# Optimization experiments

Hardware: AMD Instinct MI355X
Metric: run time of the kernel (lower is better)

## Reference

```python
import jax, jax.numpy as jnp
import numpy as np
from jax import lax

GAMMA = 2        # unused in forward (kept for fidelity to source)
PW = 10.0
THRESHOLD = 1.0
ERODE = 3
BACKZERO = 0

B, C, D, H, W = 2, 1, 128, 256, 256


def setup_inputs() -> dict:
    key = jax.random.key(0)
    k1, k2 = jax.random.split(key)
    inp = jax.random.normal(k1, (B, C, D, H, W), dtype=jnp.float32)
    tgt = jax.random.uniform(k2, (B, C, D, H, W), dtype=jnp.float32)
    return {"input": inp, "target": tgt}


def _box_sum_3d(x, r):
    # All-ones (2r+1)^3 conv3d with padding=r == sliding-window sum (shape-preserving).
    k = 2 * r + 1
    return lax.reduce_window(
        x, 0.0, lax.add,
        window_dimensions=(1, 1, k, k, k),
        window_strides=(1, 1, 1, 1, 1),
        padding=[(0, 0), (0, 0), (r, r), (r, r), (r, r)],
    )


def reference(input, target):
    # weight = clamp(target, 0, threshold); zero out voxels exactly at threshold
    w = jnp.clip(target, 0.0, THRESHOLD)
    w = w - THRESHOLD * (w == THRESHOLD).astype(jnp.float32)
    # box-filter "erosion" then binarize
    w = _box_sum_3d(w, ERODE)
    w = (w > 0).astype(jnp.float32)
    w = 1.0 + w * PW
    if BACKZERO != 0:
        mask = (input < 0).astype(jnp.float32) * (target == 0).astype(jnp.float32)
        w = w * (1.0 - mask)
    loss = jnp.abs(target - input) * w
    return jnp.mean(loss)
```

## Files before the change

### kernel.cpp

```cpp
#include <hip/hip_runtime.h>
#include <stdint.h>

#define BB 2
#define DD 128
#define HH 256
#define WW 256
static constexpr int64_t N = (int64_t)BB * DD * HH * WW;
static constexpr int WPR    = WW / 64;
static constexpr int NWORDS = BB * DD * HH * WPR;
static constexpr int RBLOCKS = 4096;

__device__ __forceinline__ uint64_t shfl_xor_u64(uint64_t v, int lanemask) {
    int lo = __shfl_xor((int)(uint32_t)v, lanemask, 64);
    int hi = __shfl_xor((int)(v >> 32), lanemask, 64);
    return ((uint64_t)(uint32_t)hi << 32) | (uint32_t)lo;
}

__global__ __launch_bounds__(256) void mask_xdil(const float* __restrict__ tgt,
                                                 uint64_t* __restrict__ mask) {
    const int wave = threadIdx.x >> 6;
    const int lane = threadIdx.x & 63;
    const int row  = blockIdx.x * 4 + wave;

    float4 t = ((const float4*)(tgt + (int64_t)row * WW))[lane];
    unsigned nib = 0;
    nib |= (t.x > 0.0f && t.x < 1.0f) ? 1u : 0u;
    nib |= (t.y > 0.0f && t.y < 1.0f) ? 2u : 0u;
    nib |= (t.z > 0.0f && t.z < 1.0f) ? 4u : 0u;
    nib |= (t.w > 0.0f && t.w < 1.0f) ? 8u : 0u;

    unsigned L = (unsigned)__shfl_up((int)nib, 1, 64);
    unsigned R = (unsigned)__shfl_down((int)nib, 1, 64);
    if (lane == 0)  L = 0;
    if (lane == 63) R = 0;

    const unsigned m = L | (nib << 4) | (R << 8);
    unsigned dil = 0;
    #pragma unroll
    for (int j = 0; j < 4; j++)
        dil |= ((m & (0x7Fu << (j + 1))) ? 1u : 0u) << j;

    uint64_t x = dil;
    #pragma unroll
    for (int s = 0; s < 4; s++) {
        const int sh = 4 << s;
        uint64_t p = shfl_xor_u64(x, 1 << s);
        x = (lane & (1 << s)) ? (p | (x << sh)) : (x | (p << sh));
    }
    if ((lane & 15) == 0)
        mask[(int64_t)row * WPR + (lane >> 4)] = x;
}

__global__ __launch_bounds__(256) void yz_dil(const uint64_t* __restrict__ in,
                                              uint64_t* __restrict__ out) {
    __shared__ uint64_t raw[22][23];
    __shared__ uint64_t yd[22][17];
    const int ty = threadIdx.x & 15;
    const int tz = threadIdx.x >> 4;
    const int y0 = blockIdx.x * 16;
    const int z0 = blockIdx.y * 16;
    const int b  = blockIdx.z >> 2;
    const int wx = blockIdx.z & 3;

    for (int idx = threadIdx.x; idx < 22 * 22; idx += 256) {
        const int zz = idx / 22, yy = idx % 22;
        const int gz = z0 - 3 + zz, gy = y0 - 3 + yy;
        uint64_t v = 0;
        if (gz >= 0 && gz < DD && gy >= 0 && gy < HH)
            v = in[(((int64_t)(b * DD + gz)) * HH + gy) * WPR + wx];
        raw[zz][yy] = v;
    }
    __syncthreads();

    for (int idx = threadIdx.x; idx < 22 * 16; idx += 256) {
        const int zz = idx >> 4, yy = idx & 15;
        uint64_t v = 0;
        #pragma unroll
        for (int d = 0; d < 7; d++) v |= raw[zz][yy + d];
        yd[zz][yy] = v;
    }
    __syncthreads();

    uint64_t v = 0;
    #pragma unroll
    for (int d = 0; d < 7; d++) v |= yd[tz + d][ty];
    out[(((int64_t)(b * DD + z0 + tz)) * HH + y0 + ty) * WPR + wx] = v;
}

__global__ __launch_bounds__(256) void reduce_loss(const float* __restrict__ inp,
                                                   const float* __restrict__ tgt,
                                                   const uint64_t* __restrict__ mask,
                                                   double* __restrict__ partials) {
    const int64_t nvec = N / 4;
    const int64_t stride = (int64_t)RBLOCKS * 256;
    float local = 0.0f;
    for (int64_t i = (int64_t)blockIdx.x * 256 + threadIdx.x; i < nvec; i += stride) {
        float4 a = ((const float4*)inp)[i];
        float4 t = ((const float4*)tgt)[i];
        uint64_t w = mask[i >> 4];
        unsigned nib = (unsigned)(w >> ((i & 15) * 4)) & 0xFu;
        float s;
        s  = fabsf(t.x - a.x) * ((nib & 1u) ? 11.0f : 1.0f);
        s += fabsf(t.y - a.y) * ((nib & 2u) ? 11.0f : 1.0f);
        s += fabsf(t.z - a.z) * ((nib & 4u) ? 11.0f : 1.0f);
        s += fabsf(t.w - a.w) * ((nib & 8u) ? 11.0f : 1.0f);
        local += s;
    }
    #pragma unroll
    for (int off = 32; off > 0; off >>= 1)
        local += __shfl_down(local, off, 64);
    __shared__ float wsum[4];
    const int lane = threadIdx.x & 63;
    const int wv   = threadIdx.x >> 6;
    if (lane == 0) wsum[wv] = local;
    __syncthreads();
    if (threadIdx.x == 0)
        partials[blockIdx.x] = (double)(wsum[0] + wsum[1] + wsum[2] + wsum[3]);
}

__global__ __launch_bounds__(1024) void finalize(const double* __restrict__ partials,
                                                 float* __restrict__ out) {
    double local = 0.0;
    for (int i = threadIdx.x; i < RBLOCKS; i += 1024) local += partials[i];
    #pragma unroll
    for (int off = 32; off > 0; off >>= 1)
        local += __shfl_down(local, off, 64);
    __shared__ double ws[16];
    const int lane = threadIdx.x & 63;
    const int wv   = threadIdx.x >> 6;
    if (lane == 0) ws[wv] = local;
    __syncthreads();
    if (threadIdx.x == 0) {
        double s = 0.0;
        #pragma unroll
        for (int k = 0; k < 16; k++) s += ws[k];
        out[0] = (float)(s / (double)N);
    }
}

extern "C" void kernel_launch(void* const* d_in, const int* in_sizes, int n_in,
                              void* d_out, int out_size, void* d_ws, size_t ws_size,
                              hipStream_t stream) {
    const float* inp = (const float*)d_in[0];
    const float* tgt = (const float*)d_in[1];
    float* out = (float*)d_out;

    double*   partials = (double*)d_ws;
    uint64_t* mask0 = (uint64_t*)((char*)d_ws + 64 * 1024);
    uint64_t* mask1 = mask0 + NWORDS;

    mask_xdil<<<NWORDS / 16, 256, 0, stream>>>(tgt, mask0);
    yz_dil<<<dim3(HH / 16, DD / 16, BB * WPR), 256, 0, stream>>>(mask0, mask1);
    reduce_loss<<<RBLOCKS, 256, 0, stream>>>(inp, tgt, mask1, partials);
    finalize<<<1, 1024, 0, stream>>>(partials, out);
}
```

Before: 151.6 us.

## Rewrite weighted loss as 11*total minus 10*unmasked sum, fusing reductions

```diff
diff --git a/kernel.cpp b/kernel.cpp
--- a/kernel.cpp
+++ b/kernel.cpp
@@ -8,7 +8,8 @@
 static constexpr int64_t N = (int64_t)BB * DD * HH * WW;
 static constexpr int WPR    = WW / 64;
 static constexpr int NWORDS = BB * DD * HH * WPR;
-static constexpr int RBLOCKS = 4096;
+static constexpr int K1_BLOCKS = NWORDS / 16;
+static constexpr int K2_BLOCKS = (HH / 16) * (DD / 16) * (BB * WPR);
 
 __device__ __forceinline__ uint64_t shfl_xor_u64(uint64_t v, int lanemask) {
     int lo = __shfl_xor((int)(uint32_t)v, lanemask, 64);
@@ -16,13 +17,21 @@
     return ((uint64_t)(uint32_t)hi << 32) | (uint32_t)lo;
 }
 
-__global__ __launch_bounds__(256) void mask_xdil(const float* __restrict__ tgt,
-                                                 uint64_t* __restrict__ mask) {
+__global__ __launch_bounds__(256) void mask_xdil_sum(const float* __restrict__ tgt,
+                                                     const float* __restrict__ inp,
+                                                     uint64_t* __restrict__ mask,
+                                                     double* __restrict__ p0) {
     const int wave = threadIdx.x >> 6;
     const int lane = threadIdx.x & 63;
     const int row  = blockIdx.x * 4 + wave;
 
-    float4 t = ((const float4*)(tgt + (int64_t)row * WW))[lane];
+    const int64_t base = (int64_t)row * WW;
+    float4 t = ((const float4*)(tgt + base))[lane];
+    float4 a = ((const float4*)(inp + base))[lane];
+
+    float s = fabsf(t.x - a.x) + fabsf(t.y - a.y)
+            + fabsf(t.z - a.z) + fabsf(t.w - a.w);
+
     unsigned nib = 0;
     nib |= (t.x > 0.0f && t.x < 1.0f) ? 1u : 0u;
     nib |= (t.y > 0.0f && t.y < 1.0f) ? 2u : 0u;
@@ -42,17 +51,28 @@
 
     uint64_t x = dil;
     #pragma unroll
-    for (int s = 0; s < 4; s++) {
-        const int sh = 4 << s;
-        uint64_t p = shfl_xor_u64(x, 1 << s);
-        x = (lane & (1 << s)) ? (p | (x << sh)) : (x | (p << sh));
+    for (int st = 0; st < 4; st++) {
+        const int sh = 4 << st;
+        uint64_t p = shfl_xor_u64(x, 1 << st);
+        x = (lane & (1 << st)) ? (p | (x << sh)) : (x | (p << sh));
     }
     if ((lane & 15) == 0)
         mask[(int64_t)row * WPR + (lane >> 4)] = x;
+
+    #pragma unroll
+    for (int off = 32; off > 0; off >>= 1)
+        s += __shfl_down(s, off, 64);
+    __shared__ float wsum[4];
+    if (lane == 0) wsum[wave] = s;
+    __syncthreads();
+    if (threadIdx.x == 0)
+        p0[blockIdx.x] = (double)((wsum[0] + wsum[1]) + (wsum[2] + wsum[3]));
 }
 
-__global__ __launch_bounds__(256) void yz_dil(const uint64_t* __restrict__ in,
-                                              uint64_t* __restrict__ out) {
+__global__ __launch_bounds__(256) void yz_dil_reduce(const uint64_t* __restrict__ in,
+                                                     const float* __restrict__ inp,
+                                                     const float* __restrict__ tgt,
+                                                     double* __restrict__ p1) {
     __shared__ uint64_t raw[22][23];
     __shared__ uint64_t yd[22][17];
     const int ty = threadIdx.x & 15;
@@ -84,57 +104,61 @@
     uint64_t v = 0;
     #pragma unroll
     for (int d = 0; d < 7; d++) v |= yd[tz + d][ty];
-    out[(((int64_t)(b * DD + z0 + tz)) * HH + y0 + ty) * WPR + wx] = v;
+
+    float sab = 0.0f;
+    if (v != ~0ull) {
+        const int64_t wi = (((int64_t)(b * DD + z0 + tz)) * HH + y0 + ty) * WPR + wx;
+        const float4* a4 = (const float4*)inp;
+        const float4* t4 = (const float4*)tgt;
+        #pragma unroll 1
+        for (int q = 0; q < 16; q++) {
+            const unsigned nb = (unsigned)(v >> (q * 4)) & 0xFu;
+            if (nb != 0xFu) {
+                float4 aa = a4[wi * 16 + q];
+                float4 tt = t4[wi * 16 + q];
+                if (!(nb & 1u)) sab += fabsf(tt.x - aa.x);
+                if (!(nb & 2u)) sab += fabsf(tt.y - aa.y);
+                if (!(nb & 4u)) sab += fabsf(tt.z - aa.z);
+                if (!(nb & 8u)) sab += fabsf(tt.w - aa.w);
+            }
+        }
+    }
+
+    #pragma unroll
+    for (int off = 32; off > 0; off >>= 1)
+        sab += __shfl_down(sab, off, 64);
+    __shared__ float ws[4];
+    const int lane = threadIdx.x & 63;
+    const int wv   = threadIdx.x >> 6;
+    if (lane == 0) ws[wv] = sab;
+    __syncthreads();
+    if (threadIdx.x == 0) {
+        const int flat = blockIdx.x + gridDim.x * (blockIdx.y + gridDim.y * blockIdx.z);
+        p1[flat] = (double)((ws[0] + ws[1]) + (ws[2] + ws[3]));
+    }
 }
 
-__global__ __launch_bounds__(256) void reduce_loss(const float* __restrict__ inp,
-                                                   const float* __restrict__ tgt,
-                                                   const uint64_t* __restrict__ mask,
-                                                   double* __restrict__ partials) {
-    const int64_t nvec = N / 4;
-    const int64_t stride = (int64_t)RBLOCKS * 256;
-    float local = 0.0f;
-    for (int64_t i = (int64_t)blockIdx.x * 256 + threadIdx.x; i < nvec; i += stride) {
-        float4 a = ((const float4*)inp)[i];
-        float4 t = ((const float4*)tgt)[i];
-        uint64_t w = mask[i >> 4];
-        unsigned nib = (unsigned)(w >> ((i & 15) * 4)) & 0xFu;
-        float s;
-        s  = fabsf(t.x - a.x) * ((nib & 1u) ? 11.0f : 1.0f);
-        s += fabsf(t.y - a.y) * ((nib & 2u) ? 11.0f : 1.0f);
-        s += fabsf(t.z - a.z) * ((nib & 4u) ? 11.0f : 1.0f);
-        s += fabsf(t.w - a.w) * ((nib & 8u) ? 11.0f : 1.0f);
-        local += s;
+__global__ __launch_bounds__(1024) void finalize(const double* __restrict__ p0,
+                                                 const double* __restrict__ p1,
+                                                 float* __restrict__ out) {
+    double s0 = 0.0, sa = 0.0;
+    for (int i = threadIdx.x; i < K1_BLOCKS; i += 1024) s0 += p0[i];
+    for (int i = threadIdx.x; i < K2_BLOCKS; i += 1024) sa += p1[i];
+    #pragma unroll
+    for (int off = 32; off > 0; off >>= 1) {
+        s0 += __shfl_down(s0, off, 64);
+        sa += __shfl_down(sa, off, 64);
     }
-    #pragma unroll
-    for (int off = 32; off > 0; off >>= 1)
-        local += __shfl_down(local, off, 64);
-    __shared__ float wsum[4];
+    __shared__ double w0[16], wa[16];
     const int lane = threadIdx.x & 63;
     const int wv   = threadIdx.x >> 6;
-    if (lane == 0) wsum[wv] = local;
-    __syncthreads();
-    if (threadIdx.x == 0)
-        partials[blockIdx.x] = (double)(wsum[0] + wsum[1] + wsum[2] + wsum[3]);
-}
-
-__global__ __launch_bounds__(1024) void finalize(const double* __restrict__ partials,
-                                                 float* __restrict__ out) {
-    double local = 0.0;
-    for (int i = threadIdx.x; i < RBLOCKS; i += 1024) local += partials[i];
-    #pragma unroll
-    for (int off = 32; off > 0; off >>= 1)
-        local += __shfl_down(local, off, 64);
-    __shared__ double ws[16];
-    const int lane = threadIdx.x & 63;
-    const int wv   = threadIdx.x >> 6;
-    if (lane == 0) ws[wv] = local;
+    if (lane == 0) { w0[wv] = s0; wa[wv] = sa; }
     __syncthreads();
     if (threadIdx.x == 0) {
-        double s = 0.0;
+        double S0 = 0.0, SA = 0.0;
         #pragma unroll
-        for (int k = 0; k < 16; k++) s += ws[k];
-        out[0] = (float)(s / (double)N);
+        for (int k = 0; k < 16; k++) { S0 += w0[k]; SA += wa[k]; }
+        out[0] = (float)((11.0 * S0 - 10.0 * SA) / (double)N);
     }
 }
 
@@ -145,12 +169,11 @@
     const float* tgt = (const float*)d_in[1];
     float* out = (float*)d_out;
 
-    double*   partials = (double*)d_ws;
-    uint64_t* mask0 = (uint64_t*)((char*)d_ws + 64 * 1024);
-    uint64_t* mask1 = mask0 + NWORDS;
+    double*   p0    = (double*)d_ws;
+    double*   p1    = (double*)((char*)d_ws + 144 * 1024);
+    uint64_t* mask0 = (uint64_t*)((char*)d_ws + 256 * 1024);
 
-    mask_xdil<<<NWORDS / 16, 256, 0, stream>>>(tgt, mask0);
-    yz_dil<<<dim3(HH / 16, DD / 16, BB * WPR), 256, 0, stream>>>(mask0, mask1);
-    reduce_loss<<<RBLOCKS, 256, 0, stream>>>(inp, tgt, mask1, partials);
-    finalize<<<1, 1024, 0, stream>>>(partials, out);
+    mask_xdil_sum<<<K1_BLOCKS, 256, 0, stream>>>(tgt, inp, mask0, p0);
+    yz_dil_reduce<<<dim3(HH / 16, DD / 16, BB * WPR), 256, 0, stream>>>(mask0, inp, tgt, p1);
+    finalize<<<1, 1024, 0, stream>>>(p0, p1, out);
 }
```

New measurement: 148.7 us. Within noise of the previous version (-1.9%).
